# Kernel tuning notes

Measured on AMD Instinct MI355X. Metric: run time of the kernel, lower is better.

The kernel has to match this reference:

```python
import jax, jax.numpy as jnp
import numpy as np

N = 50000      # nodes
F = 128        # feature_dim
H = 128        # hidden_dim
E = 1_600_000  # edges
G = 64         # graphs in batch
A = 8          # n_actions


def setup_inputs() -> dict:
    key = jax.random.key(0)
    ks = jax.random.split(key, 12)
    s = 0.05
    return {
        "x": jax.random.normal(ks[0], (N, F), jnp.float32),
        "edge_attr": jax.random.uniform(ks[1], (E, 1), jnp.float32),
        "W_e1": jax.random.normal(ks[2], (3, 1), jnp.float32) * s,
        "b_e1": jnp.zeros((1,), jnp.float32),
        "W_e2": jax.random.normal(ks[3], (1, 1), jnp.float32) * s,
        "b_e2": jnp.zeros((1,), jnp.float32),
        "W_gcn": jax.random.normal(ks[4], (F, H), jnp.float32) * s,
        "b_gcn": jnp.zeros((H,), jnp.float32),
        "W2": jax.random.normal(ks[5], (H, H), jnp.float32) * s,
        "b2": jnp.zeros((H,), jnp.float32),
        "W3": jax.random.normal(ks[6], (H, A), jnp.float32) * s,
        "b3": jnp.zeros((A,), jnp.float32),
        "edge_index": jax.random.randint(ks[7], (2, E), 0, N, jnp.int64),
        "batch": jnp.sort(jax.random.randint(ks[8], (N,), 0, G, jnp.int64)),
    }


def reference(x, edge_attr, W_e1, b_e1, W_e2, b_e2, W_gcn, b_gcn, W2, b2, W3, b3, edge_index, batch):
    # edge MLP: input is [src, dst, edge_attr] per edge -> (E, 3)
    e_feat = jnp.concatenate([edge_index.T.astype(x.dtype), edge_attr], axis=1)
    h = jax.nn.relu(e_feat @ W_e1 + b_e1)
    w = jax.nn.sigmoid(h @ W_e2 + b_e2)[:, 0]  # (E,)

    # GCNConv: add self-loops (weight 1), symmetric normalization
    loop = jnp.arange(N)
    row = jnp.concatenate([edge_index[0], loop])      # source
    col = jnp.concatenate([edge_index[1], loop])      # target
    w_all = jnp.concatenate([w, jnp.ones((N,), w.dtype)])
    deg = jax.ops.segment_sum(w_all, col, num_segments=N)
    safe_deg = jnp.where(deg > 0, deg, 1.0)
    dis = jnp.where(deg > 0, 1.0 / jnp.sqrt(safe_deg), 0.0)  # deg^-1/2, inf->0
    norm = dis[row] * w_all * dis[col]                # (E+N,)

    xw = x @ W_gcn                                    # (N, H)
    msg = norm[:, None] * xw[row]                     # (E+N, H) gather
    conv = jax.ops.segment_sum(msg, col, num_segments=N) + b_gcn  # scatter
    h1 = jax.nn.relu(conv)

    # global_mean_pool over batch index
    sums = jax.ops.segment_sum(h1, batch, num_segments=G)
    cnt = jax.ops.segment_sum(jnp.ones((N,), h1.dtype), batch, num_segments=G)
    pooled = sums / jnp.maximum(cnt, 1.0)[:, None]    # (G, H)

    h2 = jax.nn.relu(pooled @ W2 + b2)
    return h2 @ W3 + b3                               # (G, A)
```

## Files before the change

kernel.cpp:

```cpp
#include <hip/hip_runtime.h>
#include <hip/hip_fp16.h>
#include <math.h>

#define GB 64
#define AD 8
#define NC2 256
#define BSH 6
#define BS  64
#define NBMAX 1024

typedef _Float16 half8 __attribute__((ext_vector_type(8)));
typedef float    f32x4 __attribute__((ext_vector_type(4)));
typedef float    f32x2 __attribute__((ext_vector_type(2)));

__global__ __launch_bounds__(512) void k_hist2(const int* __restrict__ ei,
                                               int* __restrict__ H2,
                                               int E, int ce, int NB) {
    __shared__ int h[NBMAX];
    int c = blockIdx.x;
    for (int b = threadIdx.x; b < NB; b += 512) h[b] = 0;
    __syncthreads();
    int e0 = c * ce, e1 = min(e0 + ce, E);
    int nv = (e1 - e0) & ~3;
    const int4* dst4 = (const int4*)(ei + E + e0);
    for (int v = threadIdx.x; v < (nv >> 2); v += 512) {
        int4 d = dst4[v];
        atomicAdd(&h[d.x >> BSH], 1);
        atomicAdd(&h[d.y >> BSH], 1);
        atomicAdd(&h[d.z >> BSH], 1);
        atomicAdd(&h[d.w >> BSH], 1);
    }
    for (int e = e0 + nv + threadIdx.x; e < e1; e += 512)
        atomicAdd(&h[ei[E + e] >> BSH], 1);
    __syncthreads();
    for (int b = threadIdx.x; b < NB; b += 512)
        H2[(size_t)c * NB + b] = h[b];
}

__global__ __launch_bounds__(256) void k_cscan(int* __restrict__ H2,
                                               int* __restrict__ cntB,
                                               int NB, int nc) {
    __shared__ int ssum[256];
    int b = blockIdx.x;
    int t = threadIdx.x;
    int v = (t < nc) ? H2[(size_t)t * NB + b] : 0;
    ssum[t] = v;
    __syncthreads();
    for (int s = 1; s < 256; s <<= 1) {
        int tmp = (t >= s) ? ssum[t - s] : 0;
        __syncthreads();
        ssum[t] += tmp;
        __syncthreads();
    }
    if (t < nc) H2[(size_t)t * NB + b] = ssum[t] - v;
    if (t == 255) cntB[b] = ssum[255];
}

__global__ __launch_bounds__(1024) void k_bscan(const int* __restrict__ cntB,
                                                int* __restrict__ bb,
                                                int* __restrict__ rowptr,
                                                float* __restrict__ psum,
                                                int NB, int n, int E) {
    __shared__ int sm[1024];
    int t = threadIdx.x;
    for (int z = t; z < GB * 128 + GB; z += 1024) psum[z] = 0.0f;
    int v = (t < NB) ? cntB[t] : 0;
    sm[t] = v;
    __syncthreads();
    for (int s = 1; s < 1024; s <<= 1) {
        int tmp = (t >= s) ? sm[t - s] : 0;
        __syncthreads();
        sm[t] += tmp;
        __syncthreads();
    }
    if (t < NB) bb[t] = sm[t] - v;
    if (t == NB - 1) bb[NB] = sm[t];
    if (t == 0) rowptr[n] = E;
}

__global__ __launch_bounds__(512) void k_fill2(const int* __restrict__ ei,
                                               const float* __restrict__ attr,
                                               const float* __restrict__ W_e1,
                                               const float* __restrict__ b_e1,
                                               const float* __restrict__ W_e2,
                                               const float* __restrict__ b_e2,
                                               const int* __restrict__ bb,
                                               const int* __restrict__ H2,
                                               int2* __restrict__ rec,
                                               int E, int ce, int NB) {
    __shared__ int off[NBMAX];
    int c = blockIdx.x;
    for (int b = threadIdx.x; b < NB; b += 512)
        off[b] = bb[b] + H2[(size_t)c * NB + b];
    __syncthreads();
    float w1s = W_e1[0], w1d = W_e1[1], w1a = W_e1[2], bb1 = b_e1[0];
    float w2 = W_e2[0], bb2 = b_e2[0];
    int e0 = c * ce, e1 = min(e0 + ce, E);
    int nv = (e1 - e0) & ~3;
    const int4*   src4 = (const int4*)(ei + e0);
    const int4*   dst4 = (const int4*)(ei + E + e0);
    const float4* att4 = (const float4*)(attr + e0);
    for (int v = threadIdx.x; v < (nv >> 2); v += 512) {
        int4 sv = src4[v];
        int4 dv = dst4[v];
        float4 av = att4[v];
        int   ss[4] = {sv.x, sv.y, sv.z, sv.w};
        int   dd[4] = {dv.x, dv.y, dv.z, dv.w};
        float aa[4] = {av.x, av.y, av.z, av.w};
        #pragma unroll
        for (int k = 0; k < 4; k++) {
            float h = fmaxf((float)ss[k] * w1s + (float)dd[k] * w1d + aa[k] * w1a + bb1, 0.0f);
            float w = 1.0f / (1.0f + expf(-(h * w2 + bb2)));
            int pos = atomicAdd(&off[dd[k] >> BSH], 1);
            int2 rv;
            rv.x = ss[k] | ((dd[k] & (BS - 1)) << 16);
            rv.y = __float_as_int(w);
            rec[pos] = rv;
        }
    }
    for (int e = e0 + nv + threadIdx.x; e < e1; e += 512) {
        int d = ei[E + e];
        int s = ei[e];
        float h = fmaxf((float)s * w1s + (float)d * w1d + attr[e] * w1a + bb1, 0.0f);
        float w = 1.0f / (1.0f + expf(-(h * w2 + bb2)));
        int pos = atomicAdd(&off[d >> BSH], 1);
        int2 rv;
        rv.x = s | ((d & (BS - 1)) << 16);
        rv.y = __float_as_int(w);
        rec[pos] = rv;
    }
}

__global__ __launch_bounds__(256) void k_bucket(const int2* __restrict__ rec,
                                                const int* __restrict__ bb,
                                                unsigned int* __restrict__ rec3,
                                                int* __restrict__ rowptr,
                                                float* __restrict__ dis, int n) {
    __shared__ int   cntL[BS];
    __shared__ float degL[BS];
    __shared__ int   pfx[BS];
    __shared__ int   cnt2[BS];
    int b = blockIdx.x;
    int t = threadIdx.x;
    if (t < BS) { cntL[t] = 0; degL[t] = 1.0f; cnt2[t] = 0; }
    __syncthreads();
    int s0 = bb[b], s1 = bb[b + 1];
    for (int j = s0 + t; j < s1; j += 256) {
        int2 rv = rec[j];
        int dl = (rv.x >> 16) & (BS - 1);
        atomicAdd(&cntL[dl], 1);
        atomicAdd(&degL[dl], __int_as_float(rv.y));
    }
    __syncthreads();
    if (t == 0) {
        int acc = 0;
        for (int k = 0; k < BS; k++) { pfx[k] = acc; acc += cntL[k]; }
    }
    __syncthreads();
    int lo = b << BSH;
    if (t < BS) {
        int i = lo + t;
        if (i < n) {
            rowptr[i] = s0 + pfx[t];
            dis[i] = rsqrtf(degL[t]);
        }
    }
    for (int j = s0 + t; j < s1; j += 256) {
        int2 rv = rec[j];
        int dl = (rv.x >> 16) & (BS - 1);
        int r = atomicAdd(&cnt2[dl], 1);
        unsigned int hh = (unsigned int)__half_as_ushort(
                              __float2half(__int_as_float(rv.y)));
        rec3[s0 + pfx[dl] + r] = (unsigned int)(rv.x & 0xFFFF) | (hh << 16);
    }
}

__global__ __launch_bounds__(256) void k_xw(const float* __restrict__ x,
                                            const float* __restrict__ Wg,
                                            const float* __restrict__ dis,
                                            __half* __restrict__ xwh, int n) {
    __shared__ _Float16 Wh[128 * 136];
    int tid = threadIdx.x;
    for (int idx = tid; idx < 128 * 128; idx += 256) {
        int k = idx >> 7, c = idx & 127;
        Wh[c * 136 + k] = (_Float16)Wg[idx];
    }
    __syncthreads();

    int lane = tid & 63;
    int w = tid >> 6;
    int n16 = lane & 15;
    int quad = lane >> 4;

    #pragma unroll
    for (int hf = 0; hf < 2; hf++) {
        int r0 = blockIdx.x * 128 + hf * 64 + w * 16;
        if (r0 >= n) break;
        int arow = min(r0 + n16, n - 1);
        const float* xrow = x + (size_t)arow * 128;

        f32x4 acc[8];
        #pragma unroll
        for (int nt = 0; nt < 8; nt++) acc[nt] = (f32x4){0.f, 0.f, 0.f, 0.f};

        #pragma unroll
        for (int kk = 0; kk < 4; kk++) {
            int k0 = kk * 32 + quad * 8;
            float4 f0 = *(const float4*)(xrow + k0);
            float4 f1 = *(const float4*)(xrow + k0 + 4);
            half8 a;
            a[0] = (_Float16)f0.x; a[1] = (_Float16)f0.y;
            a[2] = (_Float16)f0.z; a[3] = (_Float16)f0.w;
            a[4] = (_Float16)f1.x; a[5] = (_Float16)f1.y;
            a[6] = (_Float16)f1.z; a[7] = (_Float16)f1.w;
            #pragma unroll
            for (int nt = 0; nt < 8; nt++) {
                half8 b = *(const half8*)&Wh[(nt * 16 + n16) * 136 + k0];
                acc[nt] = __builtin_amdgcn_mfma_f32_16x16x32_f16(a, b, acc[nt], 0, 0, 0);
            }
        }

        #pragma unroll
        for (int r = 0; r < 4; r++) {
            int row = r0 + quad * 4 + r;
            if (row < n) {
                float dv = dis[row];
                #pragma unroll
                for (int nt = 0; nt < 8; nt++)
                    xwh[(size_t)row * 128 + nt * 16 + n16] = __float2half(acc[nt][r] * dv);
            }
        }
    }
}

__global__ __launch_bounds__(256) void k_gather(const unsigned int* __restrict__ rec3,
                                                const int* __restrict__ rowptr,
                                                const float* __restrict__ dis,
                                                const __half* __restrict__ xh,
                                                const float* __restrict__ bg,
                                                __half* __restrict__ conv, int n) {
    int wave = threadIdx.x >> 6;
    int lane = threadIdx.x & 63;
    int g = lane >> 4;
    int q = lane & 15;
    int i = blockIdx.x * 4 + wave;
    if (i >= n) return;
    int st = rowptr[i];
    int m = rowptr[i + 1] - st;
    float di = dis[i];

    f32x2 acc2[4];
    {
        uint4 sr = *(const uint4*)(xh + (size_t)i * 128 + q * 8);
        const __half2* hp = (const __half2*)&sr;
        float sc = (g == 0) ? 1.0f : 0.0f;
        #pragma unroll
        for (int k = 0; k < 4; k++) {
            float2 f = __half22float2(hp[k]);
            acc2[k] = (f32x2){sc * f.x, sc * f.y};
        }
    }

    unsigned int rvcur = 0u;
    if (lane < m) rvcur = rec3[st + lane];

    for (int base = 0; base < m; base += 64) {
        int kk = min(64, m - base);
        unsigned int rv = rvcur;
        int nb = base + 64;
        unsigned int rvn = 0u;
        if (nb < m && lane < m - nb) rvn = rec3[st + nb + lane];
        rvcur = rvn;

        int jn = (kk + 3) >> 2;
        for (int j = 0; j < jn; j += 4) {
            int b4 = 4 * j + g;
            unsigned int rj0 = (unsigned int)__builtin_amdgcn_ds_bpermute((b4 + 0) << 2, (int)rv);
            unsigned int rj1 = (unsigned int)__builtin_amdgcn_ds_bpermute((b4 + 4) << 2, (int)rv);
            unsigned int rj2 = (unsigned int)__builtin_amdgcn_ds_bpermute((b4 + 8) << 2, (int)rv);
            unsigned int rj3 = (unsigned int)__builtin_amdgcn_ds_bpermute((b4 + 12) << 2, (int)rv);
            float cf0 = __half2float(__ushort_as_half((unsigned short)(rj0 >> 16)));
            float cf1 = __half2float(__ushort_as_half((unsigned short)(rj1 >> 16)));
            float cf2 = __half2float(__ushort_as_half((unsigned short)(rj2 >> 16)));
            float cf3 = __half2float(__ushort_as_half((unsigned short)(rj3 >> 16)));
            uint4 rw0 = *(const uint4*)(xh + (size_t)(rj0 & 0xFFFF) * 128 + q * 8);
            uint4 rw1 = *(const uint4*)(xh + (size_t)(rj1 & 0xFFFF) * 128 + q * 8);
            uint4 rw2 = *(const uint4*)(xh + (size_t)(rj2 & 0xFFFF) * 128 + q * 8);
            uint4 rw3 = *(const uint4*)(xh + (size_t)(rj3 & 0xFFFF) * 128 + q * 8);
            const __half2* p0 = (const __half2*)&rw0;
            const __half2* p1 = (const __half2*)&rw1;
            const __half2* p2 = (const __half2*)&rw2;
            const __half2* p3 = (const __half2*)&rw3;
            #pragma unroll
            for (int k = 0; k < 4; k++) {
                float2 f0 = __half22float2(p0[k]);
                acc2[k] += cf0 * (f32x2){f0.x, f0.y};
            }
            #pragma unroll
            for (int k = 0; k < 4; k++) {
                float2 f1 = __half22float2(p1[k]);
                acc2[k] += cf1 * (f32x2){f1.x, f1.y};
            }
            #pragma unroll
            for (int k = 0; k < 4; k++) {
                float2 f2 = __half22float2(p2[k]);
                acc2[k] += cf2 * (f32x2){f2.x, f2.y};
            }
            #pragma unroll
            for (int k = 0; k < 4; k++) {
                float2 f3 = __half22float2(p3[k]);
                acc2[k] += cf3 * (f32x2){f3.x, f3.y};
            }
        }
    }

    float acc[8];
    #pragma unroll
    for (int k = 0; k < 4; k++) {
        acc[2 * k]     = acc2[k][0];
        acc[2 * k + 1] = acc2[k][1];
    }
    #pragma unroll
    for (int k = 0; k < 8; k++) {
        acc[k] += __shfl_xor(acc[k], 16);
        acc[k] += __shfl_xor(acc[k], 32);
    }
    if (g == 0) {
        float4 b0 = *(const float4*)(bg + q * 8);
        float4 b1 = *(const float4*)(bg + q * 8 + 4);
        const float* bp = (const float*)&b0;
        float v[8];
        #pragma unroll
        for (int k = 0; k < 4; k++) v[k] = fmaxf(di * acc[k] + bp[k], 0.0f);
        bp = (const float*)&b1;
        #pragma unroll
        for (int k = 0; k < 4; k++) v[4 + k] = fmaxf(di * acc[4 + k] + bp[k], 0.0f);
        __half2 h[4];
        #pragma unroll
        for (int k = 0; k < 4; k++)
            h[k] = __halves2half2(__float2half(v[2 * k]), __float2half(v[2 * k + 1]));
        uint4 o;
        o.x = *(unsigned int*)&h[0];
        o.y = *(unsigned int*)&h[1];
        o.z = *(unsigned int*)&h[2];
        o.w = *(unsigned int*)&h[3];
        *(uint4*)(conv + (size_t)i * 128 + q * 8) = o;
    }
}

__device__ __forceinline__ int lbound(const int* __restrict__ a, int n, int v) {
    int lo = 0, hi = n;
    while (lo < hi) {
        int mid = (lo + hi) >> 1;
        if (a[mid] < v) lo = mid + 1; else hi = mid;
    }
    return lo;
}

__global__ __launch_bounds__(256) void k_pool(const __half* __restrict__ h1,
                                              const int* __restrict__ batch,
                                              float* __restrict__ psum,
                                              float* __restrict__ pcnt, int n) {
    int g = blockIdx.x, ch = blockIdx.y;
    int t = threadIdx.x;
    int s = lbound(batch, n, g);
    int e = lbound(batch, n, g + 1);
    int rq = t >> 6, q = t & 63;
    float ax = 0.0f, ay = 0.0f;
    for (int i = s + ch * 4 + rq; i < e; i += 16) {
        __half2 hv = *(const __half2*)(h1 + (size_t)i * 128 + 2 * q);
        float2 f = __half22float2(hv);
        ax += f.x; ay += f.y;
    }
    __shared__ float2 sm[256];
    sm[t] = make_float2(ax, ay);
    __syncthreads();
    if (t < 64) {
        float2 a0 = sm[t], a1 = sm[t + 64], a2 = sm[t + 128], a3 = sm[t + 192];
        atomicAdd(&psum[g * 128 + 2 * q],     a0.x + a1.x + a2.x + a3.x);
        atomicAdd(&psum[g * 128 + 2 * q + 1], a0.y + a1.y + a2.y + a3.y);
    }
    if (ch == 0 && t == 0) pcnt[g] = (float)(e - s);
}

__global__ __launch_bounds__(128) void k_head(const float* __restrict__ psum,
                                              const float* __restrict__ pcnt,
                                              const float* __restrict__ W2,
                                              const float* __restrict__ b2,
                                              const float* __restrict__ W3,
                                              const float* __restrict__ b3,
                                              float* __restrict__ out) {
    __shared__ float pl[128];
    __shared__ float h2s[128];
    int g = blockIdx.x;
    int t = threadIdx.x;
    float c = fmaxf(pcnt[g], 1.0f);
    pl[t] = psum[g * 128 + t] / c;
    __syncthreads();
    float acc = b2[t];
    for (int k = 0; k < 128; k++) acc += pl[k] * W2[k * 128 + t];
    h2s[t] = fmaxf(acc, 0.0f);
    __syncthreads();
    if (t < AD) {
        float o = b3[t];
        for (int k = 0; k < 128; k++) o += h2s[k] * W3[k * AD + t];
        out[g * AD + t] = o;
    }
}

extern "C" void kernel_launch(void* const* d_in, const int* in_sizes, int n_in,
                              void* d_out, int out_size, void* d_ws, size_t ws_size,
                              hipStream_t stream) {
    const float* x        = (const float*)d_in[0];
    const float* edge_attr= (const float*)d_in[1];
    const float* W_e1     = (const float*)d_in[2];
    const float* b_e1     = (const float*)d_in[3];
    const float* W_e2     = (const float*)d_in[4];
    const float* b_e2     = (const float*)d_in[5];
    const float* W_gcn    = (const float*)d_in[6];
    const float* b_gcn    = (const float*)d_in[7];
    const float* W2       = (const float*)d_in[8];
    const float* b2       = (const float*)d_in[9];
    const float* W3       = (const float*)d_in[10];
    const float* b3       = (const float*)d_in[11];
    const int*   ei       = (const int*)d_in[12];
    const int*   batch    = (const int*)d_in[13];
    float* out = (float*)d_out;

    const int E  = in_sizes[12] / 2;
    const int n  = in_sizes[13];
    const int NB = (n + BS - 1) >> BSH;
    const int ce = (((E + NC2 - 1) / NC2) + 3) & ~3;

    char* p = (char*)d_ws;
    __half* xwh   = (__half*)p;  p += (size_t)n * 128 * sizeof(__half);
    int*    H2    = (int*)p;
    __half* conv  = (__half*)p;  p += (size_t)n * 128 * sizeof(__half);
    int2*   rec   = (int2*)p;    p += (size_t)E * sizeof(int2);
    unsigned int* rec3 = (unsigned int*)p; p += (size_t)E * sizeof(unsigned int);
    float*  dis   = (float*)p;   p += (size_t)n * sizeof(float);
    float*  psum  = (float*)p;   p += (size_t)GB * 128 * sizeof(float);
    float*  pcnt  = (float*)p;   p += (size_t)GB * sizeof(float);
    int*    rowptr= (int*)p;     p += (size_t)(n + 1) * sizeof(int);
    int*    cntB  = (int*)p;     p += (size_t)NBMAX * sizeof(int);
    int*    bb    = (int*)p;     p += (size_t)(NBMAX + 1) * sizeof(int);

    k_hist2<<<NC2, 512, 0, stream>>>(ei, H2, E, ce, NB);
    k_cscan<<<NB, 256, 0, stream>>>(H2, cntB, NB, NC2);
    k_bscan<<<1, 1024, 0, stream>>>(cntB, bb, rowptr, psum, NB, n, E);
    k_fill2<<<NC2, 512, 0, stream>>>(ei, edge_attr, W_e1, b_e1, W_e2, b_e2,
                                     bb, H2, rec, E, ce, NB);
    k_bucket<<<NB, 256, 0, stream>>>(rec, bb, rec3, rowptr, dis, n);
    k_xw<<<(n + 127) / 128, 256, 0, stream>>>(x, W_gcn, dis, xwh, n);
    k_gather<<<(n + 3) / 4, 256, 0, stream>>>(rec3, rowptr, dis, xwh,
                                              b_gcn, conv, n);
    k_pool<<<dim3(GB, 4), 256, 0, stream>>>(conv, batch, psum, pcnt, n);
    k_head<<<GB, 128, 0, stream>>>(psum, pcnt, W2, b2, W3, b3, out);
}
```

Measured before the change: 227.7 us.

## Replace bucketed two-level edge sort with global atomic counting sort

```diff
diff --git a/kernel.cpp b/kernel.cpp
--- a/kernel.cpp
+++ b/kernel.cpp
@@ -4,174 +4,116 @@
 
 #define GB 64
 #define AD 8
-#define NC2 256
-#define BSH 6
-#define BS  64
-#define NBMAX 1024
 
 typedef _Float16 half8 __attribute__((ext_vector_type(8)));
 typedef float    f32x4 __attribute__((ext_vector_type(4)));
 typedef float    f32x2 __attribute__((ext_vector_type(2)));
 
-__global__ __launch_bounds__(512) void k_hist2(const int* __restrict__ ei,
-                                               int* __restrict__ H2,
-                                               int E, int ce, int NB) {
-    __shared__ int h[NBMAX];
-    int c = blockIdx.x;
-    for (int b = threadIdx.x; b < NB; b += 512) h[b] = 0;
-    __syncthreads();
-    int e0 = c * ce, e1 = min(e0 + ce, E);
-    int nv = (e1 - e0) & ~3;
-    const int4* dst4 = (const int4*)(ei + E + e0);
-    for (int v = threadIdx.x; v < (nv >> 2); v += 512) {
-        int4 d = dst4[v];
-        atomicAdd(&h[d.x >> BSH], 1);
-        atomicAdd(&h[d.y >> BSH], 1);
-        atomicAdd(&h[d.z >> BSH], 1);
-        atomicAdd(&h[d.w >> BSH], 1);
-    }
-    for (int e = e0 + nv + threadIdx.x; e < e1; e += 512)
-        atomicAdd(&h[ei[E + e] >> BSH], 1);
-    __syncthreads();
-    for (int b = threadIdx.x; b < NB; b += 512)
-        H2[(size_t)c * NB + b] = h[b];
-}
-
-__global__ __launch_bounds__(256) void k_cscan(int* __restrict__ H2,
-                                               int* __restrict__ cntB,
-                                               int NB, int nc) {
-    __shared__ int ssum[256];
-    int b = blockIdx.x;
-    int t = threadIdx.x;
-    int v = (t < nc) ? H2[(size_t)t * NB + b] : 0;
-    ssum[t] = v;
-    __syncthreads();
-    for (int s = 1; s < 256; s <<= 1) {
-        int tmp = (t >= s) ? ssum[t - s] : 0;
-        __syncthreads();
-        ssum[t] += tmp;
-        __syncthreads();
-    }
-    if (t < nc) H2[(size_t)t * NB + b] = ssum[t] - v;
-    if (t == 255) cntB[b] = ssum[255];
-}
-
-__global__ __launch_bounds__(1024) void k_bscan(const int* __restrict__ cntB,
-                                                int* __restrict__ bb,
-                                                int* __restrict__ rowptr,
-                                                float* __restrict__ psum,
-                                                int NB, int n, int E) {
-    __shared__ int sm[1024];
-    int t = threadIdx.x;
-    for (int z = t; z < GB * 128 + GB; z += 1024) psum[z] = 0.0f;
-    int v = (t < NB) ? cntB[t] : 0;
-    sm[t] = v;
-    __syncthreads();
-    for (int s = 1; s < 1024; s <<= 1) {
-        int tmp = (t >= s) ? sm[t - s] : 0;
-        __syncthreads();
-        sm[t] += tmp;
-        __syncthreads();
-    }
-    if (t < NB) bb[t] = sm[t] - v;
-    if (t == NB - 1) bb[NB] = sm[t];
-    if (t == 0) rowptr[n] = E;
-}
-
-__global__ __launch_bounds__(512) void k_fill2(const int* __restrict__ ei,
+__global__ __launch_bounds__(256) void k_init(int* __restrict__ cnt,
+                                              float* __restrict__ degw,
+                                              float* __restrict__ psum, int n) {
+    int i = blockIdx.x * 256 + threadIdx.x;
+    if (i < n) { cnt[i] = 0; degw[i] = 0.0f; }
+    if (i < GB * 128 + GB) psum[i] = 0.0f;
+}
+
+__global__ __launch_bounds__(256) void k_edgeA(const int* __restrict__ ei,
                                                const float* __restrict__ attr,
                                                const float* __restrict__ W_e1,
                                                const float* __restrict__ b_e1,
                                                const float* __restrict__ W_e2,
                                                const float* __restrict__ b_e2,
-                                               const int* __restrict__ bb,
-                                               const int* __restrict__ H2,
-                                               int2* __restrict__ rec,
-                                               int E, int ce, int NB) {
-    __shared__ int off[NBMAX];
-    int c = blockIdx.x;
-    for (int b = threadIdx.x; b < NB; b += 512)
-        off[b] = bb[b] + H2[(size_t)c * NB + b];
-    __syncthreads();
+                                               int* __restrict__ cnt,
+                                               float* __restrict__ degw,
+                                               unsigned int* __restrict__ urec, int E) {
     float w1s = W_e1[0], w1d = W_e1[1], w1a = W_e1[2], bb1 = b_e1[0];
     float w2 = W_e2[0], bb2 = b_e2[0];
-    int e0 = c * ce, e1 = min(e0 + ce, E);
-    int nv = (e1 - e0) & ~3;
-    const int4*   src4 = (const int4*)(ei + e0);
-    const int4*   dst4 = (const int4*)(ei + E + e0);
-    const float4* att4 = (const float4*)(attr + e0);
-    for (int v = threadIdx.x; v < (nv >> 2); v += 512) {
-        int4 sv = src4[v];
-        int4 dv = dst4[v];
-        float4 av = att4[v];
+    int v = blockIdx.x * 256 + threadIdx.x;
+    int nv = E >> 2;
+    if (v < nv) {
+        int4   sv = ((const int4*)ei)[v];
+        int4   dv = ((const int4*)(ei + E))[v];
+        float4 av = ((const float4*)attr)[v];
         int   ss[4] = {sv.x, sv.y, sv.z, sv.w};
         int   dd[4] = {dv.x, dv.y, dv.z, dv.w};
         float aa[4] = {av.x, av.y, av.z, av.w};
+        unsigned int uo[4];
         #pragma unroll
         for (int k = 0; k < 4; k++) {
             float h = fmaxf((float)ss[k] * w1s + (float)dd[k] * w1d + aa[k] * w1a + bb1, 0.0f);
             float w = 1.0f / (1.0f + expf(-(h * w2 + bb2)));
-            int pos = atomicAdd(&off[dd[k] >> BSH], 1);
-            int2 rv;
-            rv.x = ss[k] | ((dd[k] & (BS - 1)) << 16);
-            rv.y = __float_as_int(w);
-            rec[pos] = rv;
-        }
-    }
-    for (int e = e0 + nv + threadIdx.x; e < e1; e += 512) {
-        int d = ei[E + e];
-        int s = ei[e];
-        float h = fmaxf((float)s * w1s + (float)d * w1d + attr[e] * w1a + bb1, 0.0f);
-        float w = 1.0f / (1.0f + expf(-(h * w2 + bb2)));
-        int pos = atomicAdd(&off[d >> BSH], 1);
-        int2 rv;
-        rv.x = s | ((d & (BS - 1)) << 16);
-        rv.y = __float_as_int(w);
-        rec[pos] = rv;
-    }
-}
-
-__global__ __launch_bounds__(256) void k_bucket(const int2* __restrict__ rec,
-                                                const int* __restrict__ bb,
-                                                unsigned int* __restrict__ rec3,
-                                                int* __restrict__ rowptr,
-                                                float* __restrict__ dis, int n) {
-    __shared__ int   cntL[BS];
-    __shared__ float degL[BS];
-    __shared__ int   pfx[BS];
-    __shared__ int   cnt2[BS];
-    int b = blockIdx.x;
+            atomicAdd(&cnt[dd[k]], 1);
+            atomicAdd(&degw[dd[k]], w);
+            uo[k] = (unsigned int)(ss[k] & 0xFFFF) |
+                    ((unsigned int)__half_as_ushort(__float2half(w)) << 16);
+        }
+        uint4 o; o.x = uo[0]; o.y = uo[1]; o.z = uo[2]; o.w = uo[3];
+        ((uint4*)urec)[v] = o;
+    }
+    if (v == 0) {
+        for (int e = nv << 2; e < E; ++e) {
+            int s = ei[e], d = ei[E + e];
+            float h = fmaxf((float)s * w1s + (float)d * w1d + attr[e] * w1a + bb1, 0.0f);
+            float w = 1.0f / (1.0f + expf(-(h * w2 + bb2)));
+            atomicAdd(&cnt[d], 1);
+            atomicAdd(&degw[d], w);
+            urec[e] = (unsigned int)(s & 0xFFFF) |
+                      ((unsigned int)__half_as_ushort(__float2half(w)) << 16);
+        }
+    }
+}
+
+__global__ __launch_bounds__(1024) void k_scan(const int* __restrict__ cnt,
+                                               const float* __restrict__ degw,
+                                               int* __restrict__ rowptr,
+                                               int* __restrict__ cur,
+                                               float* __restrict__ dis,
+                                               int n, int E) {
+    __shared__ int sm[1024];
     int t = threadIdx.x;
-    if (t < BS) { cntL[t] = 0; degL[t] = 1.0f; cnt2[t] = 0; }
+    int per = (n + 1023) >> 10;
+    int a = t * per;
+    int b = min(a + per, n);
+    if (a > n) a = n;
+    int s = 0;
+    for (int i = a; i < b; ++i) s += cnt[i];
+    sm[t] = s;
     __syncthreads();
-    int s0 = bb[b], s1 = bb[b + 1];
-    for (int j = s0 + t; j < s1; j += 256) {
-        int2 rv = rec[j];
-        int dl = (rv.x >> 16) & (BS - 1);
-        atomicAdd(&cntL[dl], 1);
-        atomicAdd(&degL[dl], __int_as_float(rv.y));
-    }
-    __syncthreads();
-    if (t == 0) {
-        int acc = 0;
-        for (int k = 0; k < BS; k++) { pfx[k] = acc; acc += cntL[k]; }
-    }
-    __syncthreads();
-    int lo = b << BSH;
-    if (t < BS) {
-        int i = lo + t;
-        if (i < n) {
-            rowptr[i] = s0 + pfx[t];
-            dis[i] = rsqrtf(degL[t]);
-        }
-    }
-    for (int j = s0 + t; j < s1; j += 256) {
-        int2 rv = rec[j];
-        int dl = (rv.x >> 16) & (BS - 1);
-        int r = atomicAdd(&cnt2[dl], 1);
-        unsigned int hh = (unsigned int)__half_as_ushort(
-                              __float2half(__int_as_float(rv.y)));
-        rec3[s0 + pfx[dl] + r] = (unsigned int)(rv.x & 0xFFFF) | (hh << 16);
+    for (int st = 1; st < 1024; st <<= 1) {
+        int tmp = (t >= st) ? sm[t - st] : 0;
+        __syncthreads();
+        sm[t] += tmp;
+        __syncthreads();
+    }
+    int run = sm[t] - s;
+    for (int i = a; i < b; ++i) {
+        rowptr[i] = run;
+        cur[i]    = run;
+        run += cnt[i];
+        dis[i] = rsqrtf(1.0f + degw[i]);
+    }
+    if (t == 1023) rowptr[n] = E;
+}
+
+__global__ __launch_bounds__(256) void k_edgeC(const int* __restrict__ ei,
+                                               const unsigned int* __restrict__ urec,
+                                               int* __restrict__ cur,
+                                               unsigned int* __restrict__ rec3, int E) {
+    int v = blockIdx.x * 256 + threadIdx.x;
+    int nv = E >> 2;
+    if (v < nv) {
+        int4  dv = ((const int4*)(ei + E))[v];
+        uint4 uv = ((const uint4*)urec)[v];
+        int p0 = atomicAdd(&cur[dv.x], 1); rec3[p0] = uv.x;
+        int p1 = atomicAdd(&cur[dv.y], 1); rec3[p1] = uv.y;
+        int p2 = atomicAdd(&cur[dv.z], 1); rec3[p2] = uv.z;
+        int p3 = atomicAdd(&cur[dv.w], 1); rec3[p3] = uv.w;
+    }
+    if (v == 0) {
+        for (int e = nv << 2; e < E; ++e) {
+            int p = atomicAdd(&cur[ei[E + e]], 1);
+            rec3[p] = urec[e];
+        }
     }
 }
 
@@ -429,31 +371,30 @@
 
     const int E  = in_sizes[12] / 2;
     const int n  = in_sizes[13];
-    const int NB = (n + BS - 1) >> BSH;
-    const int ce = (((E + NC2 - 1) / NC2) + 3) & ~3;
 
     char* p = (char*)d_ws;
     __half* xwh   = (__half*)p;  p += (size_t)n * 128 * sizeof(__half);
-    int*    H2    = (int*)p;
     __half* conv  = (__half*)p;  p += (size_t)n * 128 * sizeof(__half);
-    int2*   rec   = (int2*)p;    p += (size_t)E * sizeof(int2);
+    unsigned int* urec = (unsigned int*)p; p += (size_t)E * sizeof(unsigned int);
     unsigned int* rec3 = (unsigned int*)p; p += (size_t)E * sizeof(unsigned int);
+    int*    cnt   = (int*)p;     p += (size_t)n * sizeof(int);
+    int*    cur   = (int*)p;     p += (size_t)n * sizeof(int);
+    float*  degw  = (float*)p;   p += (size_t)n * sizeof(float);
     float*  dis   = (float*)p;   p += (size_t)n * sizeof(float);
     float*  psum  = (float*)p;   p += (size_t)GB * 128 * sizeof(float);
     float*  pcnt  = (float*)p;   p += (size_t)GB * sizeof(float);
     int*    rowptr= (int*)p;     p += (size_t)(n + 1) * sizeof(int);
-    int*    cntB  = (int*)p;     p += (size_t)NBMAX * sizeof(int);
-    int*    bb    = (int*)p;     p += (size_t)(NBMAX + 1) * sizeof(int);
-
-    k_hist2<<<NC2, 512, 0, stream>>>(ei, H2, E, ce, NB);
-    k_cscan<<<NB, 256, 0, stream>>>(H2, cntB, NB, NC2);
-    k_bscan<<<1, 1024, 0, stream>>>(cntB, bb, rowptr, psum, NB, n, E);
-    k_fill2<<<NC2, 512, 0, stream>>>(ei, edge_attr, W_e1, b_e1, W_e2, b_e2,
-                                     bb, H2, rec, E, ce, NB);
-    k_bucket<<<NB, 256, 0, stream>>>(rec, bb, rec3, rowptr, dis, n);
-    k_xw<<<(n + 127) / 128, 256, 0, stream>>>(x, W_gcn, dis, xwh, n);
+
+    const int nb4 = ((E >> 2) + 255) / 256;
+
+    k_init <<<(n + 255) / 256, 256, 0, stream>>>(cnt, degw, psum, n);
+    k_edgeA<<<nb4, 256, 0, stream>>>(ei, edge_attr, W_e1, b_e1, W_e2, b_e2,
+                                     cnt, degw, urec, E);
+    k_scan <<<1, 1024, 0, stream>>>(cnt, degw, rowptr, cur, dis, n, E);
+    k_edgeC<<<nb4, 256, 0, stream>>>(ei, urec, cur, rec3, E);
+    k_xw   <<<(n + 127) / 128, 256, 0, stream>>>(x, W_gcn, dis, xwh, n);
     k_gather<<<(n + 3) / 4, 256, 0, stream>>>(rec3, rowptr, dis, xwh,
                                               b_gcn, conv, n);
-    k_pool<<<dim3(GB, 4), 256, 0, stream>>>(conv, batch, psum, pcnt, n);
-    k_head<<<GB, 128, 0, stream>>>(psum, pcnt, W2, b2, W3, b3, out);
-}
+    k_pool <<<dim3(GB, 4), 256, 0, stream>>>(conv, batch, psum, pcnt, n);
+    k_head <<<GB, 128, 0, stream>>>(psum, pcnt, W2, b2, W3, b3, out);
+}
```

New measurement: 643.2 us. 183% more time.
